# Kernel tuning notes

Measured on AMD Instinct MI355X. Metric: run time of the kernel, lower is better.

Reference implementation:

```python
import jax, jax.numpy as jnp
import numpy as np

NUM_ITERATIONS = 3


def squash(t, axis=-1):
    # scale = |t|^2 / (1 + |t|^2); out = scale * t / |t|  (matches torch source exactly)
    norm = jnp.sum(t * t, axis=axis, keepdims=True)
    scale = norm / (1.0 + norm)
    return scale * t / jnp.sqrt(norm)


def setup_inputs() -> dict:
    key = jax.random.key(0)
    k_u, k_w = jax.random.split(key)
    B, K, R, M, P = 1024, 2, 2336, 4, 16
    u = jax.random.normal(k_u, (B, R, M), dtype=jnp.float32)
    W = jax.random.normal(k_w, (K, R, M, P), dtype=jnp.float32)
    return {"u": u, "W": W}


def reference(u, W):
    # u: [B, R, M]; W: [K, R, M, P]
    # torch: matmul(u[:,None,:,None,:], W) -> [B,K,R,1,P]; we drop the singleton dim.
    u_ji = jnp.einsum('brm,krmp->bkrp', u, W)  # [B, K, R, P]
    b = jnp.zeros_like(u_ji)
    v = None
    for i in range(NUM_ITERATIONS):
        c = jax.nn.softmax(b, axis=2)                      # softmax over routes
        v = squash(jnp.sum(c * u_ji, axis=2, keepdims=True))  # [B, K, 1, P]
        if i != NUM_ITERATIONS - 1:
            b = b + jnp.sum(u_ji * v, axis=-1, keepdims=True)  # agreement, broadcasts over P
    v = jnp.squeeze(v, axis=2)                 # [B, K, P]
    classes = jnp.sqrt(jnp.sum(v * v, axis=-1))  # [B, K]
    return classes
```

## Files before the change

### kernel.cpp

```cpp
#include <hip/hip_runtime.h>
#include <hip/hip_fp16.h>
#include <math.h>


#define THREADS 512
#define NWAVE 8
#define RR 2336
#define KK 2

#if __has_builtin(__builtin_amdgcn_fdot2)
typedef _Float16 h2v __attribute__((ext_vector_type(2)));
static __device__ __forceinline__ float dot2h(__half2 a, __half2 b, float c) {
    h2v av, bv;
    __builtin_memcpy(&av, &a, 4);
    __builtin_memcpy(&bv, &b, 4);
    return __builtin_amdgcn_fdot2(av, bv, c, false);
}
#else
static __device__ __forceinline__ float dot2h(__half2 a, __half2 b, float c) {
    float2 fa = __half22float2(a), fb = __half22float2(b);
    return fmaf(fa.x, fb.x, fmaf(fa.y, fb.y, c));
}
#endif

#define DPP_XOR1 0xB1
#define DPP_XOR2 0x4E
#define DPP_ROR4 0x124
#define DPP_ROR8 0x128

template <int CTRL>
static __device__ __forceinline__ float dpp_addf(float x) {
    const int y = __builtin_amdgcn_update_dpp(0, __float_as_int(x), CTRL, 0xf, 0xf, true);
    return x + __int_as_float(y);
}
static __device__ __forceinline__ float swz16_addf(float x) {
    const int y = __builtin_amdgcn_ds_swizzle(__float_as_int(x), 0x401f);
    return x + __int_as_float(y);
}
#if __has_builtin(__builtin_amdgcn_permlane32_swap)
static __device__ __forceinline__ float pl32_addf(float x) {
    typedef unsigned uv2 __attribute__((ext_vector_type(2)));
    const uv2 r = __builtin_amdgcn_permlane32_swap(__float_as_uint(x), __float_as_uint(x),
                                                   false, false);
    return __uint_as_float(r[0]) + __uint_as_float(r[1]);
}
#else
static __device__ __forceinline__ float pl32_addf(float x) { return x + __shfl_xor(x, 32); }
#endif

__global__ __launch_bounds__(256)
void w_repack_kernel(const float* __restrict__ W, __half2* __restrict__ Wt)
{
    const int n = KK * RR * 8;
    for (int j = blockIdx.x * 256 + threadIdx.x; j < n; j += gridDim.x * 256) {
        const int p2 = j & 7;
        const int rk = j >> 3;
        const float* wp = W + (size_t)rk * 64;
        const float x0 = wp[0*16 + 2*p2],     x1 = wp[1*16 + 2*p2];
        const float x2 = wp[2*16 + 2*p2],     x3 = wp[3*16 + 2*p2];
        const float y0 = wp[0*16 + 2*p2 + 1], y1 = wp[1*16 + 2*p2 + 1];
        const float y2 = wp[2*16 + 2*p2 + 1], y3 = wp[3*16 + 2*p2 + 1];
        __half2* o = Wt + (size_t)j * 4;
        o[0] = __floats2half2_rn(x0, x1);
        o[1] = __floats2half2_rn(x2, x3);
        o[2] = __floats2half2_rn(y0, y1);
        o[3] = __floats2half2_rn(y2, y3);
    }
}

#define STREAM_COMP(base, i, uu, wv)                                   \
    {                                                                  \
        const int r = (base) + (i) * 64 + rbase;                       \
        const __half2 u01 = __floats2half2_rn(uu.x, uu.y);             \
        const __half2 u23 = __floats2half2_rn(uu.z, uu.w);             \
        const __half2* hm = (const __half2*)&wv;                       \
        const float ax = dot2h(u01, hm[0], dot2h(u23, hm[1], 0.0f));   \
        const float ay = dot2h(u01, hm[2], dot2h(u23, hm[3], 0.0f));   \
        sA += ax; sB += ay;                                            \
        *(__half2*)(uji + r * 16 + p2 * 2) = __floats2half2_rn(ax, ay); \
    }

#define SWEEP_STEP(rw)                                                     \
    {                                                                      \
        const __half2* hp = (const __half2*)&(rw);                         \
        float d = dot2h(hp[0], v2[0], dot2h(hp[1], v2[1],                  \
                  dot2h(hp[2], v2[2], dot2h(hp[3], v2[3], 0.0f))));        \
        d = dpp_addf<DPP_XOR1>(d);             \
        const float e = __expf(d);           \
        se += e;                                                           \
        { const float2 f0 = __half22float2(hp[0]);                         \
          s8[0] = fmaf(f0.x, e, s8[0]); s8[1] = fmaf(f0.y, e, s8[1]); }    \
        { const float2 f1 = __half22float2(hp[1]);                         \
          s8[2] = fmaf(f1.x, e, s8[2]); s8[3] = fmaf(f1.y, e, s8[3]); }    \
        { const float2 f2 = __half22float2(hp[2]);                         \
          s8[4] = fmaf(f2.x, e, s8[4]); s8[5] = fmaf(f2.y, e, s8[5]); }    \
        { const float2 f3 = __half22float2(hp[3]);                         \
          s8[6] = fmaf(f3.x, e, s8[6]); s8[7] = fmaf(f3.y, e, s8[7]); }    \
    }

__global__ __launch_bounds__(THREADS, 2)
void caps_routing_kernel(const float* __restrict__ u,
                         const __half2* __restrict__ Wt,
                         float* __restrict__ out)
{
    __shared__ __align__(16) __half uji[RR * 16];
    __shared__ __align__(16) float  red[2][NWAVE][20];
    __shared__ __align__(16) float  vrow[2][16];

    const int bi   = blockIdx.x;
    const int b    = bi >> 1;
    const int k    = bi & 1;
    const int tid  = threadIdx.x;
    const int lane = tid & 63;
    const int wave = tid >> 6;
    const int p2   = lane & 7;
    const int g    = lane >> 3;

    const float4* __restrict__ u4p = (const float4*)u;
    const float4* __restrict__ w4t = (const float4*)Wt + (size_t)k * RR * 8 + p2;

    float sA = 0.0f, sB = 0.0f;
    {
        const int rbase = wave * 8 + g;
        float4 uuA_n = u4p[b * RR + rbase];
        float4 wvA_n = w4t[(size_t)rbase * 8];
        float4 uuB_n = u4p[b * RR + 768 + rbase];
        float4 wvB_n = w4t[(size_t)(768 + rbase) * 8];
        float4 uuC_n = u4p[b * RR + 1536 + rbase];
        float4 wvC_n = w4t[(size_t)(1536 + rbase) * 8];
        #pragma unroll 3
        for (int i = 0; i < 12; ++i) {
            const float4 uuA = uuA_n, wvA = wvA_n;
            const float4 uuB = uuB_n, wvB = wvB_n;
            const float4 uuC = uuC_n, wvC = wvC_n;
            if (i + 1 < 12) {
                const int ra = (i + 1) * 64 + rbase;
                uuA_n = u4p[b * RR + ra];
                wvA_n = w4t[(size_t)ra * 8];
                const int rb = 768 + (i + 1) * 64 + rbase;
                uuB_n = u4p[b * RR + rb];
                wvB_n = w4t[(size_t)rb * 8];
                const int rc = 1536 + (i + 1) * 64 + rbase;
                uuC_n = u4p[b * RR + rc];
                wvC_n = w4t[(size_t)rc * 8];
            }
            STREAM_COMP(0,    i, uuA, wvA)
            STREAM_COMP(768,  i, uuB, wvB)
            STREAM_COMP(1536, i, uuC, wvC)
        }
        if (wave < 4) {
            const int r = 2304 + rbase;
            const float4 uu = u4p[b * RR + r];
            const float4 wv = w4t[(size_t)r * 8];
            const __half2 u01 = __floats2half2_rn(uu.x, uu.y);
            const __half2 u23 = __floats2half2_rn(uu.z, uu.w);
            const __half2* hm = (const __half2*)&wv;
            const float ax = dot2h(u01, hm[0], dot2h(u23, hm[1], 0.0f));
            const float ay = dot2h(u01, hm[2], dot2h(u23, hm[3], 0.0f));
            sA += ax; sB += ay;
            *(__half2*)(uji + r * 16 + p2 * 2) = __floats2half2_rn(ax, ay);
        }
    }
    sA = dpp_addf<DPP_ROR8>(sA);  sB = dpp_addf<DPP_ROR8>(sB);
    sA = swz16_addf(sA);          sB = swz16_addf(sB);
    sA = pl32_addf(sA);           sB = pl32_addf(sB);
    if (lane < 8) {
        red[0][wave][2 * p2]     = sA;
        red[0][wave][2 * p2 + 1] = sB;
    }
    __syncthreads();

    float vcum_s;
    {
        float col = 0.0f;
        #pragma unroll
        for (int w = 0; w < NWAVE; ++w) col += red[0][w][lane & 15];
        float nr = col * col;
        nr = dpp_addf<DPP_XOR1>(nr);
        nr = dpp_addf<DPP_XOR2>(nr);
        nr = dpp_addf<DPP_ROR4>(nr);
        nr = dpp_addf<DPP_ROR8>(nr);
        const float inv  = 1.0f / (float)RR;
        const float norm = nr * inv * inv;
        const float f    = sqrtf(norm) / (1.0f + norm);
        vcum_s = col * inv * f;
        if (lane < 16) vrow[0][lane] = vcum_s;
    }

    #pragma unroll 1
    for (int it = 1; it < 3; ++it) {
        const int buf = it & 1;

        __half2 v2[4];
        {
            const float2* vp = (const float2*)vrow[buf ^ 1];
            #pragma unroll
            for (int q = 0; q < 4; ++q) {
                const float2 pv = vp[(lane & 1) * 4 + q];
                v2[q] = __floats2half2_rn(pv.x, pv.y);
            }
        }

        float4 raw[9], raw9;
        {
            const int rb = wave * 32 + (lane >> 1);
            #pragma unroll
            for (int s = 0; s < 9; ++s)
                raw[s] = *(const float4*)((const char*)uji + (s * 256 + rb) * 32 + (lane & 1) * 16);
            raw9 = *(const float4*)((const char*)uji + (2304 + (lane >> 1)) * 32 + (lane & 1) * 16);
        }

        float s8[8] = {0, 0, 0, 0, 0, 0, 0, 0};
        float se = 0.0f;
        #pragma unroll
        for (int s = 0; s < 9; ++s) SWEEP_STEP(raw[s])
        if (wave == 0) SWEEP_STEP(raw9)

        #pragma unroll
        for (int i = 0; i < 8; ++i) {
            s8[i] = dpp_addf<DPP_XOR2>(s8[i]);
            s8[i] = dpp_addf<DPP_ROR4>(s8[i]);
            s8[i] = dpp_addf<DPP_ROR8>(s8[i]);
            s8[i] = swz16_addf(s8[i]);
            s8[i] = pl32_addf(s8[i]);
        }
        se = dpp_addf<DPP_XOR2>(se);
        se = dpp_addf<DPP_ROR4>(se);
        se = dpp_addf<DPP_ROR8>(se);
        se = swz16_addf(se);
        se = pl32_addf(se);

        if (lane < 2) {
            *(float4*)&red[buf][wave][(lane & 1) * 8]     = make_float4(s8[0], s8[1], s8[2], s8[3]);
            *(float4*)&red[buf][wave][(lane & 1) * 8 + 4] = make_float4(s8[4], s8[5], s8[6], s8[7]);
            if (lane == 0) red[buf][wave][16] = se;
        }
        __syncthreads();

        {
            float col = 0.0f, set = 0.0f;
            #pragma unroll
            for (int w = 0; w < NWAVE; ++w) {
                col += red[buf][w][lane & 15];
                set += red[buf][w][16];
            }
            float nr = col * col;
            nr = dpp_addf<DPP_XOR1>(nr);
            nr = dpp_addf<DPP_XOR2>(nr);
            nr = dpp_addf<DPP_ROR4>(nr);
            nr = dpp_addf<DPP_ROR8>(nr);
            const float inv  = 1.0f / set;
            const float norm = nr * inv * inv;
            if (it == 1) {
                const float f = sqrtf(norm) / (1.0f + norm);
                vcum_s += col * inv * f;
                if (lane < 16) vrow[1][lane] = vcum_s;
            } else if (wave == 0 && lane == 0) {
                out[b * KK + k] = norm / (1.0f + norm);
            }
        }
    }
}

extern "C" void kernel_launch(void* const* d_in, const int* in_sizes, int n_in,
                              void* d_out, int out_size, void* d_ws, size_t ws_size,
                              hipStream_t stream) {
    const float* u = (const float*)d_in[0];
    const float* W = (const float*)d_in[1];
    float* out = (float*)d_out;
    __half2* Wt = (__half2*)d_ws;

    w_repack_kernel<<<dim3(256), dim3(256), 0, stream>>>(W, Wt);
    caps_routing_kernel<<<dim3(2048), dim3(THREADS), 0, stream>>>(u, Wt, out);
}
```

Before: 121.3 us.

## Drop W repack kernel and read fp32 W directly with fp32 FMAs

Removes the separate fp16 repack kernel and its launch, and the main kernel now loads W straight from the original fp32 layout as four float2 loads per route. The u·W projection is computed in fp32 with FMAs instead of packed fp16 dot products. The stream loop is restructured from three interleaved 768-route segments to two 1152-route segments over 18 iterations. In exchange, each block reads twice as many W bytes through scattered 8-byte loads rather than one 16-byte coalesced load, which may raise L2 traffic.

```diff
diff --git a/kernel.cpp b/kernel.cpp
--- a/kernel.cpp
+++ b/kernel.cpp
@@ -48,36 +48,15 @@
 static __device__ __forceinline__ float pl32_addf(float x) { return x + __shfl_xor(x, 32); }
 #endif
 
-__global__ __launch_bounds__(256)
-void w_repack_kernel(const float* __restrict__ W, __half2* __restrict__ Wt)
-{
-    const int n = KK * RR * 8;
-    for (int j = blockIdx.x * 256 + threadIdx.x; j < n; j += gridDim.x * 256) {
-        const int p2 = j & 7;
-        const int rk = j >> 3;
-        const float* wp = W + (size_t)rk * 64;
-        const float x0 = wp[0*16 + 2*p2],     x1 = wp[1*16 + 2*p2];
-        const float x2 = wp[2*16 + 2*p2],     x3 = wp[3*16 + 2*p2];
-        const float y0 = wp[0*16 + 2*p2 + 1], y1 = wp[1*16 + 2*p2 + 1];
-        const float y2 = wp[2*16 + 2*p2 + 1], y3 = wp[3*16 + 2*p2 + 1];
-        __half2* o = Wt + (size_t)j * 4;
-        o[0] = __floats2half2_rn(x0, x1);
-        o[1] = __floats2half2_rn(x2, x3);
-        o[2] = __floats2half2_rn(y0, y1);
-        o[3] = __floats2half2_rn(y2, y3);
-    }
-}
-
-#define STREAM_COMP(base, i, uu, wv)                                   \
-    {                                                                  \
-        const int r = (base) + (i) * 64 + rbase;                       \
-        const __half2 u01 = __floats2half2_rn(uu.x, uu.y);             \
-        const __half2 u23 = __floats2half2_rn(uu.z, uu.w);             \
-        const __half2* hm = (const __half2*)&wv;                       \
-        const float ax = dot2h(u01, hm[0], dot2h(u23, hm[1], 0.0f));   \
-        const float ay = dot2h(u01, hm[2], dot2h(u23, hm[3], 0.0f));   \
-        sA += ax; sB += ay;                                            \
-        *(__half2*)(uji + r * 16 + p2 * 2) = __floats2half2_rn(ax, ay); \
+#define STREAM_F32(base, i, uu, w0, w1, w2, w3)                               \
+    {                                                                         \
+        const int r = (base) + (i) * 64 + rbase;                              \
+        const float ax = fmaf(uu.x, w0.x, fmaf(uu.y, w1.x,                    \
+                         fmaf(uu.z, w2.x, uu.w * w3.x)));                     \
+        const float ay = fmaf(uu.x, w0.y, fmaf(uu.y, w1.y,                    \
+                         fmaf(uu.z, w2.y, uu.w * w3.y)));                     \
+        sA += ax; sB += ay;                                                   \
+        *(__half2*)(uji + r * 16 + p2 * 2) = __floats2half2_rn(ax, ay);       \
     }
 
 #define SWEEP_STEP(rw)                                                     \
@@ -100,7 +79,7 @@
 
 __global__ __launch_bounds__(THREADS, 2)
 void caps_routing_kernel(const float* __restrict__ u,
-                         const __half2* __restrict__ Wt,
+                         const float* __restrict__ W,
                          float* __restrict__ out)
 {
     __shared__ __align__(16) __half uji[RR * 16];
@@ -117,46 +96,70 @@
     const int g    = lane >> 3;
 
     const float4* __restrict__ u4p = (const float4*)u;
-    const float4* __restrict__ w4t = (const float4*)Wt + (size_t)k * RR * 8 + p2;
+    const float* __restrict__ Wf = W + (size_t)k * RR * 64 + 2 * p2;
 
     float sA = 0.0f, sB = 0.0f;
     {
         const int rbase = wave * 8 + g;
         float4 uuA_n = u4p[b * RR + rbase];
-        float4 wvA_n = w4t[(size_t)rbase * 8];
-        float4 uuB_n = u4p[b * RR + 768 + rbase];
-        float4 wvB_n = w4t[(size_t)(768 + rbase) * 8];
-        float4 uuC_n = u4p[b * RR + 1536 + rbase];
-        float4 wvC_n = w4t[(size_t)(1536 + rbase) * 8];
+        float2 wA0_n, wA1_n, wA2_n, wA3_n;
+        {
+            const float* wp = Wf + (size_t)rbase * 64;
+            wA0_n = *(const float2*)(wp);
+            wA1_n = *(const float2*)(wp + 16);
+            wA2_n = *(const float2*)(wp + 32);
+            wA3_n = *(const float2*)(wp + 48);
+        }
+        float4 uuB_n = u4p[b * RR + 1152 + rbase];
+        float2 wB0_n, wB1_n, wB2_n, wB3_n;
+        {
+            const float* wp = Wf + (size_t)(1152 + rbase) * 64;
+            wB0_n = *(const float2*)(wp);
+            wB1_n = *(const float2*)(wp + 16);
+            wB2_n = *(const float2*)(wp + 32);
+            wB3_n = *(const float2*)(wp + 48);
+        }
         #pragma unroll 3
-        for (int i = 0; i < 12; ++i) {
-            const float4 uuA = uuA_n, wvA = wvA_n;
-            const float4 uuB = uuB_n, wvB = wvB_n;
-            const float4 uuC = uuC_n, wvC = wvC_n;
-            if (i + 1 < 12) {
+        for (int i = 0; i < 18; ++i) {
+            const float4 uuA = uuA_n;
+            const float2 wA0 = wA0_n, wA1 = wA1_n, wA2 = wA2_n, wA3 = wA3_n;
+            const float4 uuB = uuB_n;
+            const float2 wB0 = wB0_n, wB1 = wB1_n, wB2 = wB2_n, wB3 = wB3_n;
+            if (i + 1 < 18) {
                 const int ra = (i + 1) * 64 + rbase;
                 uuA_n = u4p[b * RR + ra];
-                wvA_n = w4t[(size_t)ra * 8];
-                const int rb = 768 + (i + 1) * 64 + rbase;
+                {
+                    const float* wp = Wf + (size_t)ra * 64;
+                    wA0_n = *(const float2*)(wp);
+                    wA1_n = *(const float2*)(wp + 16);
+                    wA2_n = *(const float2*)(wp + 32);
+                    wA3_n = *(const float2*)(wp + 48);
+                }
+                const int rb = 1152 + ra;
                 uuB_n = u4p[b * RR + rb];
-                wvB_n = w4t[(size_t)rb * 8];
-                const int rc = 1536 + (i + 1) * 64 + rbase;
-                uuC_n = u4p[b * RR + rc];
-                wvC_n = w4t[(size_t)rc * 8];
-            }
-            STREAM_COMP(0,    i, uuA, wvA)
-            STREAM_COMP(768,  i, uuB, wvB)
-            STREAM_COMP(1536, i, uuC, wvC)
+                {
+                    const float* wp = Wf + (size_t)rb * 64;
+                    wB0_n = *(const float2*)(wp);
+                    wB1_n = *(const float2*)(wp + 16);
+                    wB2_n = *(const float2*)(wp + 32);
+                    wB3_n = *(const float2*)(wp + 48);
+                }
+            }
+            STREAM_F32(0,    i, uuA, wA0, wA1, wA2, wA3)
+            STREAM_F32(1152, i, uuB, wB0, wB1, wB2, wB3)
         }
         if (wave < 4) {
             const int r = 2304 + rbase;
             const float4 uu = u4p[b * RR + r];
-            const float4 wv = w4t[(size_t)r * 8];
-            const __half2 u01 = __floats2half2_rn(uu.x, uu.y);
-            const __half2 u23 = __floats2half2_rn(uu.z, uu.w);
-            const __half2* hm = (const __half2*)&wv;
-            const float ax = dot2h(u01, hm[0], dot2h(u23, hm[1], 0.0f));
-            const float ay = dot2h(u01, hm[2], dot2h(u23, hm[3], 0.0f));
+            const float* wp = Wf + (size_t)r * 64;
+            const float2 w0 = *(const float2*)(wp);
+            const float2 w1 = *(const float2*)(wp + 16);
+            const float2 w2 = *(const float2*)(wp + 32);
+            const float2 w3 = *(const float2*)(wp + 48);
+            const float ax = fmaf(uu.x, w0.x, fmaf(uu.y, w1.x,
+                             fmaf(uu.z, w2.x, uu.w * w3.x)));
+            const float ay = fmaf(uu.x, w0.y, fmaf(uu.y, w1.y,
+                             fmaf(uu.z, w2.y, uu.w * w3.y)));
             sA += ax; sB += ay;
             *(__half2*)(uji + r * 16 + p2 * 2) = __floats2half2_rn(ax, ay);
         }
@@ -268,8 +271,7 @@
     const float* u = (const float*)d_in[0];
     const float* W = (const float*)d_in[1];
     float* out = (float*)d_out;
-    __half2* Wt = (__half2*)d_ws;
-
-    w_repack_kernel<<<dim3(256), dim3(256), 0, stream>>>(W, Wt);
-    caps_routing_kernel<<<dim3(2048), dim3(THREADS), 0, stream>>>(u, Wt, out);
-}
+    (void)d_ws; (void)ws_size;
+
+    caps_routing_kernel<<<dim3(2048), dim3(THREADS), 0, stream>>>(u, W, out);
+}
```

After: 157.7 us. 30.1% more time.
